# Kernel optimization log

Hardware: AMD Instinct MI355X
Metric: run time of the kernel (lower is better)

The kernel has to match this reference:

```python
import jax, jax.numpy as jnp
import numpy as np

B = 64
H = 768  # hidden_dim; x is [B, H, H], split along dim 1 into Q, D of [B, H//2, H]


def setup_inputs() -> dict:
    key = jax.random.key(0)
    kx, kw, kb = jax.random.split(key, 3)
    x = jax.random.normal(kx, (B, H, H), dtype=jnp.float32)
    # nn.Linear(H, H): weight [out, in], bias [out]
    W = jax.random.normal(kw, (H, H), dtype=jnp.float32) * (1.0 / np.sqrt(H))
    b = jax.random.normal(kb, (H,), dtype=jnp.float32) * 0.01
    return {"x": x, "W": W, "b": b}


def reference(x, W, b):
    T = H // 2
    Q = x[:, :T, :]          # [B, T, H]
    D = x[:, T:2 * T, :]     # [B, T, H]
    # Q = tanh(Linear(Q)); torch Linear: y = x @ W^T + b
    Q = jnp.tanh(jnp.einsum('bth,oh->bto', Q, W) + b)  # [B, T, H]
    D_t = jnp.swapaxes(D, 1, 2)                         # [B, H, T]
    L = jnp.einsum('bth,bsh->bts', Q, D)                # [B, T, T]
    A_Q = jnp.swapaxes(jax.nn.softmax(L, axis=1), 1, 2) # softmax over dim 1, then transpose -> [B, T, T]
    C_Q = jnp.matmul(D_t, A_Q)                          # [B, H, T]
    Q_t = jnp.swapaxes(Q, 1, 2)                         # [B, H, T]
    A_D = jax.nn.softmax(L, axis=2)                     # [B, T, T]
    C_D = jnp.matmul(jnp.concatenate((Q_t, C_Q), axis=1), A_D)  # [B, 2H, T]
    C_D_t = jnp.swapaxes(C_D, 1, 2)                     # [B, T, 2H]
    return jnp.concatenate((C_D_t, D), axis=2)          # [B, T, 3H]
```

## Files before the change

kernel.cpp:

```cpp
#include <hip/hip_runtime.h>


typedef __bf16 bf16x8 __attribute__((ext_vector_type(8)));
typedef __bf16 bf16x4 __attribute__((ext_vector_type(4)));
typedef float  f32x4  __attribute__((ext_vector_type(4)));

#define HH 768
#define TT 384

__device__ inline void split8(const float* __restrict__ p, bf16x8& hi, bf16x8& lo) {
    float4 f0 = *(const float4*)p;
    float4 f1 = *(const float4*)(p + 4);
    float f[8] = {f0.x, f0.y, f0.z, f0.w, f1.x, f1.y, f1.z, f1.w};
#pragma unroll
    for (int i = 0; i < 8; i++) {
        __bf16 h = (__bf16)f[i];
        hi[i] = h;
        lo[i] = (__bf16)(f[i] - (float)h);
    }
}

__device__ inline void gload16(const void* g, void* l) {
    __builtin_amdgcn_global_load_lds(
        (const __attribute__((address_space(1))) unsigned int*)g,
        (__attribute__((address_space(3))) unsigned int*)l, 16, 0, 0);
}

__global__ void prep_kernel(const float* __restrict__ x, __bf16* __restrict__ Dt,
                            float* __restrict__ out) {
    __shared__ float tile[32][33];
    int b = blockIdx.z;
    int h0 = blockIdx.x * 32, s0 = blockIdx.y * 32;
    int tx = threadIdx.x, ty = threadIdx.y;
    const float* src = x + ((size_t)b * HH + TT) * HH;
    float* outb = out + (size_t)b * TT * 2304;
#pragma unroll
    for (int j = 0; j < 4; j++) {
        int s = s0 + ty + 8 * j, h = h0 + tx;
        float v = src[(size_t)s * HH + h];
        tile[ty + 8 * j][tx] = v;
        outb[(size_t)s * 2304 + 1536 + h] = v;
    }
    __syncthreads();
    __bf16* Dtb = Dt + (size_t)b * HH * TT;
#pragma unroll
    for (int j = 0; j < 4; j++) {
        int h = h0 + ty + 8 * j, s = s0 + tx;
        Dtb[(size_t)h * TT + s] = (__bf16)tile[tx][ty + 8 * j];
    }
}

__global__ void splitW_kernel(const float* __restrict__ W, __bf16* __restrict__ Whi,
                              __bf16* __restrict__ Wlo) {
    int idx = blockIdx.x * 256 + threadIdx.x;
    bf16x8 h, l;
    split8(W + (size_t)idx * 8, h, l);
    *(bf16x8*)&Whi[(size_t)idx * 8] = h;
    *(bf16x8*)&Wlo[(size_t)idx * 8] = l;
}

__global__ __launch_bounds__(256) void gemm1_kernel(
    const float* __restrict__ x, const __bf16* __restrict__ Whi,
    const __bf16* __restrict__ Wlo, const float* __restrict__ bias,
    __bf16* __restrict__ Qhi, __bf16* __restrict__ Qlo, __bf16* __restrict__ M4) {
    __shared__ __bf16 Ah[128 * 32], Al[128 * 32], Bh[128 * 32], Bl[128 * 32];
    const int b = blockIdx.z;
    const int m_blk = blockIdx.y * 128, n_blk = blockIdx.x * 128;
    const int tid = threadIdx.x, lane = tid & 63, wave = tid >> 6;
    const int wm = wave >> 1, wn = wave & 1;
    const int r15 = lane & 15, quad = lane >> 4;
    const float* Abase = x + (size_t)b * HH * HH;
    f32x4 acc[4][4];
#pragma unroll
    for (int i = 0; i < 4; i++)
#pragma unroll
        for (int j = 0; j < 4; j++) acc[i][j] = (f32x4){0.f, 0.f, 0.f, 0.f};

    for (int k0 = 0; k0 < HH; k0 += 32) {
#pragma unroll
        for (int it = 0; it < 2; it++) {
            int c = it * 256 + tid;
            int r = c >> 2, q = c & 3;
            bf16x8 wh = *(const bf16x8*)&Whi[(size_t)(n_blk + r) * HH + k0 + q * 8];
            bf16x8 wl = *(const bf16x8*)&Wlo[(size_t)(n_blk + r) * HH + k0 + q * 8];
            *(bf16x8*)&Bh[c * 8] = wh;
            *(bf16x8*)&Bl[c * 8] = wl;
            bf16x8 h, l;
            split8(Abase + (size_t)(m_blk + r) * HH + k0 + q * 8, h, l);
            *(bf16x8*)&Ah[c * 8] = h;
            *(bf16x8*)&Al[c * 8] = l;
        }
        __syncthreads();
        bf16x8 ah[4], al[4], bh[4], bl[4];
#pragma unroll
        for (int i = 0; i < 4; i++) {
            int ra = (wm * 64 + i * 16 + r15) * 32 + quad * 8;
            ah[i] = *(const bf16x8*)&Ah[ra];
            al[i] = *(const bf16x8*)&Al[ra];
            int rb = (wn * 64 + i * 16 + r15) * 32 + quad * 8;
            bh[i] = *(const bf16x8*)&Bh[rb];
            bl[i] = *(const bf16x8*)&Bl[rb];
        }
#pragma unroll
        for (int i = 0; i < 4; i++)
#pragma unroll
            for (int j = 0; j < 4; j++) {
                acc[i][j] = __builtin_amdgcn_mfma_f32_16x16x32_bf16(ah[i], bh[j], acc[i][j], 0, 0, 0);
                acc[i][j] = __builtin_amdgcn_mfma_f32_16x16x32_bf16(ah[i], bl[j], acc[i][j], 0, 0, 0);
                acc[i][j] = __builtin_amdgcn_mfma_f32_16x16x32_bf16(al[i], bh[j], acc[i][j], 0, 0, 0);
            }
        __syncthreads();
    }
    __bf16* Qh = Qhi + (size_t)b * TT * HH;
    __bf16* Ql = Qlo + (size_t)b * TT * HH;
    __bf16* Mb = M4 + (size_t)b * 1536 * TT;
#pragma unroll
    for (int j = 0; j < 4; j++) {
        int col = n_blk + wn * 64 + j * 16 + r15;
        float bv = bias[col];
#pragma unroll
        for (int i = 0; i < 4; i++) {
            int row0 = m_blk + wm * 64 + i * 16 + quad * 4;
            bf16x4 mrow;
#pragma unroll
            for (int r = 0; r < 4; r++) {
                float v = tanhf(acc[i][j][r] + bv);
                __bf16 qh = (__bf16)v;
                Qh[(size_t)(row0 + r) * HH + col] = qh;
                Ql[(size_t)(row0 + r) * HH + col] = (__bf16)(v - (float)qh);
                mrow[r] = qh;
            }
            *(bf16x4*)&Mb[(size_t)col * TT + row0] = mrow;
        }
    }
}

__global__ __launch_bounds__(256) void gemm2_kernel(
    const __bf16* __restrict__ Qhi, const __bf16* __restrict__ Qlo,
    const float* __restrict__ x, float* __restrict__ L) {
    __shared__ __bf16 Ah[128 * 32], Al[128 * 32], Bh[128 * 32], Bl[128 * 32];
    const int b = blockIdx.z;
    const int m_blk = blockIdx.y * 128, n_blk = blockIdx.x * 128;
    const int tid = threadIdx.x, lane = tid & 63, wave = tid >> 6;
    const int wm = wave >> 1, wn = wave & 1;
    const int r15 = lane & 15, quad = lane >> 4;
    const __bf16* Qh = Qhi + (size_t)b * TT * HH;
    const __bf16* Ql = Qlo + (size_t)b * TT * HH;
    const float* Dbase = x + ((size_t)b * HH + TT) * HH;
    f32x4 acc[4][4];
#pragma unroll
    for (int i = 0; i < 4; i++)
#pragma unroll
        for (int j = 0; j < 4; j++) acc[i][j] = (f32x4){0.f, 0.f, 0.f, 0.f};

    for (int k0 = 0; k0 < HH; k0 += 32) {
#pragma unroll
        for (int it = 0; it < 2; it++) {
            int c = it * 256 + tid;
            int r = c >> 2, q = c & 3;
            bf16x8 qh8 = *(const bf16x8*)&Qh[(size_t)(m_blk + r) * HH + k0 + q * 8];
            bf16x8 ql8 = *(const bf16x8*)&Ql[(size_t)(m_blk + r) * HH + k0 + q * 8];
            *(bf16x8*)&Ah[c * 8] = qh8;
            *(bf16x8*)&Al[c * 8] = ql8;
            bf16x8 h, l;
            split8(Dbase + (size_t)(n_blk + r) * HH + k0 + q * 8, h, l);
            *(bf16x8*)&Bh[c * 8] = h;
            *(bf16x8*)&Bl[c * 8] = l;
        }
        __syncthreads();
        bf16x8 ah[4], al[4], bh[4], bl[4];
#pragma unroll
        for (int i = 0; i < 4; i++) {
            int ra = (wm * 64 + i * 16 + r15) * 32 + quad * 8;
            ah[i] = *(const bf16x8*)&Ah[ra];
            al[i] = *(const bf16x8*)&Al[ra];
            int rb = (wn * 64 + i * 16 + r15) * 32 + quad * 8;
            bh[i] = *(const bf16x8*)&Bh[rb];
            bl[i] = *(const bf16x8*)&Bl[rb];
        }
#pragma unroll
        for (int i = 0; i < 4; i++)
#pragma unroll
            for (int j = 0; j < 4; j++) {
                acc[i][j] = __builtin_amdgcn_mfma_f32_16x16x32_bf16(ah[i], bh[j], acc[i][j], 0, 0, 0);
                acc[i][j] = __builtin_amdgcn_mfma_f32_16x16x32_bf16(ah[i], bl[j], acc[i][j], 0, 0, 0);
                acc[i][j] = __builtin_amdgcn_mfma_f32_16x16x32_bf16(al[i], bh[j], acc[i][j], 0, 0, 0);
            }
        __syncthreads();
    }
    float* Lb = L + (size_t)b * TT * TT;
#pragma unroll
    for (int j = 0; j < 4; j++) {
        int col = n_blk + wn * 64 + j * 16 + r15;
#pragma unroll
        for (int i = 0; i < 4; i++) {
            int row0 = m_blk + wm * 64 + i * 16 + quad * 4;
#pragma unroll
            for (int r = 0; r < 4; r++) Lb[(size_t)(row0 + r) * TT + col] = acc[i][j][r];
        }
    }
}

__global__ void softmax_col_kernel(const float* __restrict__ L, __bf16* __restrict__ AQt) {
    int b = blockIdx.y;
    int tx = threadIdx.x, ty = threadIdx.y;
    int s = blockIdx.x * 64 + tx;
    const float* Lb = L + (size_t)b * TT * TT;
    __shared__ float red[4][64];
    float mx = -1e30f;
    for (int t = ty; t < TT; t += 4) mx = fmaxf(mx, Lb[(size_t)t * TT + s]);
    red[ty][tx] = mx;
    __syncthreads();
    mx = fmaxf(fmaxf(red[0][tx], red[1][tx]), fmaxf(red[2][tx], red[3][tx]));
    float sum = 0.f;
    for (int t = ty; t < TT; t += 4) sum += __expf(Lb[(size_t)t * TT + s] - mx);
    __syncthreads();
    red[ty][tx] = sum;
    __syncthreads();
    float inv = 1.0f / (red[0][tx] + red[1][tx] + red[2][tx] + red[3][tx]);
    __bf16* Ab = AQt + (size_t)b * TT * TT;
    for (int t = ty; t < TT; t += 4)
        Ab[(size_t)t * TT + s] = (__bf16)(__expf(Lb[(size_t)t * TT + s] - mx) * inv);
}

__global__ void softmax_row_kernel(const float* __restrict__ L, __bf16* __restrict__ ADt) {
    int b = blockIdx.y;
    int t0 = blockIdx.x * 64;
    int tx = threadIdx.x, ty = threadIdx.y;
    int tid = ty * 64 + tx;
    const float* Lb = L + (size_t)b * TT * TT;
    __shared__ __bf16 ex[64][TT];
    for (int rr = ty; rr < 64; rr += 4) {
        const float* row = Lb + (size_t)(t0 + rr) * TT;
        float v[6];
        float mx = -1e30f;
#pragma unroll
        for (int k = 0; k < 6; k++) {
            v[k] = row[tx + 64 * k];
            mx = fmaxf(mx, v[k]);
        }
#pragma unroll
        for (int off = 32; off > 0; off >>= 1) mx = fmaxf(mx, __shfl_xor(mx, off));
        float sum = 0.f;
#pragma unroll
        for (int k = 0; k < 6; k++) {
            v[k] = __expf(v[k] - mx);
            sum += v[k];
        }
#pragma unroll
        for (int off = 32; off > 0; off >>= 1) sum += __shfl_xor(sum, off);
        float inv = 1.0f / sum;
#pragma unroll
        for (int k = 0; k < 6; k++) ex[rr][tx + 64 * k] = (__bf16)(v[k] * inv);
    }
    __syncthreads();
    __bf16* Ab = ADt + (size_t)b * TT * TT;
    for (int s = tid; s < TT; s += 256) {
#pragma unroll
        for (int j = 0; j < 8; j++) {
            bf16x8 t8;
#pragma unroll
            for (int e = 0; e < 8; e++) t8[e] = ex[j * 8 + e][s];
            *(bf16x8*)&Ab[(size_t)s * TT + t0 + j * 8] = t8;
        }
    }
}

__global__ __launch_bounds__(256) void gemm3_kernel(
    const __bf16* __restrict__ Dt, const __bf16* __restrict__ AQt,
    __bf16* __restrict__ M4) {
    __shared__ __bf16 As[128 * 32], Bs[128 * 32];
    const int b = blockIdx.z;
    const int m_blk = blockIdx.y * 128, n_blk = blockIdx.x * 128;
    const int tid = threadIdx.x, lane = tid & 63, wave = tid >> 6;
    const int wm = wave >> 1, wn = wave & 1;
    const int r15 = lane & 15, quad = lane >> 4;
    const __bf16* Ab = Dt + (size_t)b * HH * TT;
    const __bf16* Bb = AQt + (size_t)b * TT * TT;
    f32x4 acc[4][4];
#pragma unroll
    for (int i = 0; i < 4; i++)
#pragma unroll
        for (int j = 0; j < 4; j++) acc[i][j] = (f32x4){0.f, 0.f, 0.f, 0.f};

    for (int k0 = 0; k0 < TT; k0 += 32) {
#pragma unroll
        for (int it = 0; it < 2; it++) {
            int c = it * 256 + tid;
            int r = c >> 2, q = c & 3;
            gload16(Ab + (size_t)(m_blk + r) * TT + k0 + q * 8, &As[c * 8]);
            gload16(Bb + (size_t)(n_blk + r) * TT + k0 + q * 8, &Bs[c * 8]);
        }
        __syncthreads();
        bf16x8 a[4], bf[4];
#pragma unroll
        for (int i = 0; i < 4; i++) {
            a[i] = *(const bf16x8*)&As[(wm * 64 + i * 16 + r15) * 32 + quad * 8];
            bf[i] = *(const bf16x8*)&Bs[(wn * 64 + i * 16 + r15) * 32 + quad * 8];
        }
#pragma unroll
        for (int i = 0; i < 4; i++)
#pragma unroll
            for (int j = 0; j < 4; j++)
                acc[i][j] = __builtin_amdgcn_mfma_f32_16x16x32_bf16(a[i], bf[j], acc[i][j], 0, 0, 0);
        __syncthreads();
    }
    __bf16* Mb = M4 + (size_t)b * 1536 * TT;
#pragma unroll
    for (int j = 0; j < 4; j++) {
        int col = n_blk + wn * 64 + j * 16 + r15;
#pragma unroll
        for (int i = 0; i < 4; i++) {
            int row0 = m_blk + wm * 64 + i * 16 + quad * 4;
#pragma unroll
            for (int r = 0; r < 4; r++)
                Mb[(size_t)(768 + row0 + r) * TT + col] = (__bf16)acc[i][j][r];
        }
    }
}

__global__ __launch_bounds__(256) void gemm4_kernel(
    const __bf16* __restrict__ ADt, const __bf16* __restrict__ M4,
    float* __restrict__ out) {
    __shared__ __bf16 As[128 * 32], Bs[128 * 32];
    const int b = blockIdx.z;
    const int m_blk = blockIdx.y * 128, n_blk = blockIdx.x * 128;
    const int tid = threadIdx.x, lane = tid & 63, wave = tid >> 6;
    const int wm = wave >> 1, wn = wave & 1;
    const int r15 = lane & 15, quad = lane >> 4;
    const __bf16* Ab = ADt + (size_t)b * TT * TT;
    const __bf16* Bb = M4 + (size_t)b * 1536 * TT;
    f32x4 acc[4][4];
#pragma unroll
    for (int i = 0; i < 4; i++)
#pragma unroll
        for (int j = 0; j < 4; j++) acc[i][j] = (f32x4){0.f, 0.f, 0.f, 0.f};

    for (int k0 = 0; k0 < TT; k0 += 32) {
#pragma unroll
        for (int it = 0; it < 2; it++) {
            int c = it * 256 + tid;
            int r = c >> 2, q = c & 3;
            gload16(Ab + (size_t)(m_blk + r) * TT + k0 + q * 8, &As[c * 8]);
            gload16(Bb + (size_t)(n_blk + r) * TT + k0 + q * 8, &Bs[c * 8]);
        }
        __syncthreads();
        bf16x8 a[4], bf[4];
#pragma unroll
        for (int i = 0; i < 4; i++) {
            a[i] = *(const bf16x8*)&As[(wm * 64 + i * 16 + r15) * 32 + quad * 8];
            bf[i] = *(const bf16x8*)&Bs[(wn * 64 + i * 16 + r15) * 32 + quad * 8];
        }
#pragma unroll
        for (int i = 0; i < 4; i++)
#pragma unroll
            for (int j = 0; j < 4; j++)
                acc[i][j] = __builtin_amdgcn_mfma_f32_16x16x32_bf16(a[i], bf[j], acc[i][j], 0, 0, 0);
        __syncthreads();
    }
    float* outb = out + (size_t)b * TT * 2304;
#pragma unroll
    for (int j = 0; j < 4; j++) {
        int col = n_blk + wn * 64 + j * 16 + r15;
#pragma unroll
        for (int i = 0; i < 4; i++) {
            int row0 = m_blk + wm * 64 + i * 16 + quad * 4;
#pragma unroll
            for (int r = 0; r < 4; r++)
                outb[(size_t)(row0 + r) * 2304 + col] = acc[i][j][r];
        }
    }
}

extern "C" void kernel_launch(void* const* d_in, const int* in_sizes, int n_in,
                              void* d_out, int out_size, void* d_ws, size_t ws_size,
                              hipStream_t stream) {
    const float* x = (const float*)d_in[0];
    const float* W = (const float*)d_in[1];
    const float* bias = (const float*)d_in[2];
    float* out = (float*)d_out;
    char* ws = (char*)d_ws;

    __bf16* Qhi = (__bf16*)(ws + 0);
    __bf16* Qlo = (__bf16*)(ws + 37748736);
    __bf16* M4 = (__bf16*)(ws + 75497472);
    __bf16* Dt = (__bf16*)(ws + 150994944);
    float* L = (float*)(ws + 188743680);
    __bf16* AQt = (__bf16*)(ws + 0);
    __bf16* ADt = (__bf16*)(ws + 37748736);
    __bf16* Whi = (__bf16*)(ws + 188743680);
    __bf16* Wlo = Whi + 768 * 768;

    prep_kernel<<<dim3(24, 12, 64), dim3(32, 8), 0, stream>>>(x, Dt, out);
    splitW_kernel<<<288, 256, 0, stream>>>(W, Whi, Wlo);
    gemm1_kernel<<<dim3(6, 3, 64), 256, 0, stream>>>(x, Whi, Wlo, bias, Qhi, Qlo, M4);
    gemm2_kernel<<<dim3(3, 3, 64), 256, 0, stream>>>(Qhi, Qlo, x, L);
    softmax_col_kernel<<<dim3(6, 64), dim3(64, 4), 0, stream>>>(L, AQt);
    softmax_row_kernel<<<dim3(6, 64), dim3(64, 4), 0, stream>>>(L, ADt);
    gemm3_kernel<<<dim3(3, 6, 64), 256, 0, stream>>>(Dt, AQt, M4);
    gemm4_kernel<<<dim3(12, 3, 64), 256, 0, stream>>>(ADt, M4, out);
}
```

Measured before the change: 815.8 us.

## Pre-split x and W into bf16 hi/lo scratch and stream via direct LDS loads

A new split kernel converts the Q half of x, the D half of x and W into bf16 hi/lo pairs once, storing them in spare regions of the output buffer and in workspace (M4, XQlo). gemm1 and gemm2 then fetch operands with global_load_lds directly into shared memory, no longer converting fp32 to bf16 inside every tile iteration. This removes repeated split work across the N-tiles and register staging of the loads. In exchange it adds an extra pass that writes and rereads scratch data, and it depends on later kernels overwriting the borrowed output regions and on M4 regions not being clobbered before use.

```diff
diff --git a/kernel.cpp b/kernel.cpp
--- a/kernel.cpp
+++ b/kernel.cpp
@@ -7,6 +7,7 @@
 
 #define HH 768
 #define TT 384
+#define OROWB 9216
 
 __device__ inline void split8(const float* __restrict__ p, bf16x8& hi, bf16x8& lo) {
     float4 f0 = *(const float4*)p;
@@ -50,18 +51,40 @@
     }
 }
 
-__global__ void splitW_kernel(const float* __restrict__ W, __bf16* __restrict__ Whi,
-                              __bf16* __restrict__ Wlo) {
+__global__ void splitX_kernel(const float* __restrict__ x, const float* __restrict__ W,
+                              char* __restrict__ outc, __bf16* __restrict__ M4,
+                              __bf16* __restrict__ XQlo) {
     int idx = blockIdx.x * 256 + threadIdx.x;
-    bf16x8 h, l;
-    split8(W + (size_t)idx * 8, h, l);
-    *(bf16x8*)&Whi[(size_t)idx * 8] = h;
-    *(bf16x8*)&Wlo[(size_t)idx * 8] = l;
+    const int NQ = 64 * 384 * 96;
+    if (idx < NQ) {
+        int hb = idx % 96, s = (idx / 96) % 384, b = idx / (96 * 384);
+        bf16x8 h, l;
+        split8(x + ((size_t)b * HH + s) * HH + hb * 8, h, l);
+        size_t o = (size_t)s * HH + hb * 8;
+        *(bf16x8*)&M4[((size_t)b * 1536 + 768) * TT + o] = h;
+        *(bf16x8*)&XQlo[(size_t)b * TT * HH + o] = l;
+    } else if (idx < 2 * NQ) {
+        int j = idx - NQ;
+        int hb = j % 96, s = (j / 96) % 384, b = j / (96 * 384);
+        bf16x8 h, l;
+        split8(x + ((size_t)b * HH + TT + s) * HH + hb * 8, h, l);
+        char* p = outc + (size_t)b * TT * OROWB + (size_t)s * OROWB + hb * 16;
+        *(bf16x8*)(p + 3072) = h;
+        *(bf16x8*)(p + 4608) = l;
+    } else {
+        int wi = idx - 2 * NQ;
+        int hb = wi % 96, o = wi / 96;
+        bf16x8 h, l;
+        split8(W + (size_t)o * HH + hb * 8, h, l);
+        char* p = outc + (size_t)o * OROWB + hb * 16;
+        *(bf16x8*)p = h;
+        *(bf16x8*)(p + 1536) = l;
+    }
 }
 
 __global__ __launch_bounds__(256) void gemm1_kernel(
-    const float* __restrict__ x, const __bf16* __restrict__ Whi,
-    const __bf16* __restrict__ Wlo, const float* __restrict__ bias,
+    const __bf16* __restrict__ XQlo, const char* __restrict__ wscr,
+    const float* __restrict__ bias,
     __bf16* __restrict__ Qhi, __bf16* __restrict__ Qlo, __bf16* __restrict__ M4) {
     __shared__ __bf16 Ah[128 * 32], Al[128 * 32], Bh[128 * 32], Bl[128 * 32];
     const int b = blockIdx.z;
@@ -69,7 +92,8 @@
     const int tid = threadIdx.x, lane = tid & 63, wave = tid >> 6;
     const int wm = wave >> 1, wn = wave & 1;
     const int r15 = lane & 15, quad = lane >> 4;
-    const float* Abase = x + (size_t)b * HH * HH;
+    const __bf16* XQh = M4 + ((size_t)b * 1536 + 768) * TT;
+    const __bf16* XQl = XQlo + (size_t)b * TT * HH;
     f32x4 acc[4][4];
 #pragma unroll
     for (int i = 0; i < 4; i++)
@@ -81,14 +105,11 @@
         for (int it = 0; it < 2; it++) {
             int c = it * 256 + tid;
             int r = c >> 2, q = c & 3;
-            bf16x8 wh = *(const bf16x8*)&Whi[(size_t)(n_blk + r) * HH + k0 + q * 8];
-            bf16x8 wl = *(const bf16x8*)&Wlo[(size_t)(n_blk + r) * HH + k0 + q * 8];
-            *(bf16x8*)&Bh[c * 8] = wh;
-            *(bf16x8*)&Bl[c * 8] = wl;
-            bf16x8 h, l;
-            split8(Abase + (size_t)(m_blk + r) * HH + k0 + q * 8, h, l);
-            *(bf16x8*)&Ah[c * 8] = h;
-            *(bf16x8*)&Al[c * 8] = l;
+            gload16(XQh + (size_t)(m_blk + r) * HH + k0 + q * 8, &Ah[c * 8]);
+            gload16(XQl + (size_t)(m_blk + r) * HH + k0 + q * 8, &Al[c * 8]);
+            const char* wrow = wscr + (size_t)(n_blk + r) * OROWB + (size_t)(k0 + q * 8) * 2;
+            gload16(wrow, &Bh[c * 8]);
+            gload16(wrow + 1536, &Bl[c * 8]);
         }
         __syncthreads();
         bf16x8 ah[4], al[4], bh[4], bl[4];
@@ -137,7 +158,7 @@
 
 __global__ __launch_bounds__(256) void gemm2_kernel(
     const __bf16* __restrict__ Qhi, const __bf16* __restrict__ Qlo,
-    const float* __restrict__ x, float* __restrict__ L) {
+    const char* __restrict__ outscr, float* __restrict__ L) {
     __shared__ __bf16 Ah[128 * 32], Al[128 * 32], Bh[128 * 32], Bl[128 * 32];
     const int b = blockIdx.z;
     const int m_blk = blockIdx.y * 128, n_blk = blockIdx.x * 128;
@@ -146,7 +167,7 @@
     const int r15 = lane & 15, quad = lane >> 4;
     const __bf16* Qh = Qhi + (size_t)b * TT * HH;
     const __bf16* Ql = Qlo + (size_t)b * TT * HH;
-    const float* Dbase = x + ((size_t)b * HH + TT) * HH;
+    const char* scr = outscr + (size_t)b * TT * OROWB;
     f32x4 acc[4][4];
 #pragma unroll
     for (int i = 0; i < 4; i++)
@@ -158,14 +179,11 @@
         for (int it = 0; it < 2; it++) {
             int c = it * 256 + tid;
             int r = c >> 2, q = c & 3;
-            bf16x8 qh8 = *(const bf16x8*)&Qh[(size_t)(m_blk + r) * HH + k0 + q * 8];
-            bf16x8 ql8 = *(const bf16x8*)&Ql[(size_t)(m_blk + r) * HH + k0 + q * 8];
-            *(bf16x8*)&Ah[c * 8] = qh8;
-            *(bf16x8*)&Al[c * 8] = ql8;
-            bf16x8 h, l;
-            split8(Dbase + (size_t)(n_blk + r) * HH + k0 + q * 8, h, l);
-            *(bf16x8*)&Bh[c * 8] = h;
-            *(bf16x8*)&Bl[c * 8] = l;
+            gload16(Qh + (size_t)(m_blk + r) * HH + k0 + q * 8, &Ah[c * 8]);
+            gload16(Ql + (size_t)(m_blk + r) * HH + k0 + q * 8, &Al[c * 8]);
+            const char* drow = scr + (size_t)(n_blk + r) * OROWB + (size_t)(k0 + q * 8) * 2;
+            gload16(drow + 3072, &Bh[c * 8]);
+            gload16(drow + 4608, &Bl[c * 8]);
         }
         __syncthreads();
         bf16x8 ah[4], al[4], bh[4], bl[4];
@@ -388,13 +406,12 @@
     float* L = (float*)(ws + 188743680);
     __bf16* AQt = (__bf16*)(ws + 0);
     __bf16* ADt = (__bf16*)(ws + 37748736);
-    __bf16* Whi = (__bf16*)(ws + 188743680);
-    __bf16* Wlo = Whi + 768 * 768;
+    __bf16* XQlo = (__bf16*)(ws + 188743680);
 
     prep_kernel<<<dim3(24, 12, 64), dim3(32, 8), 0, stream>>>(x, Dt, out);
-    splitW_kernel<<<288, 256, 0, stream>>>(W, Whi, Wlo);
-    gemm1_kernel<<<dim3(6, 3, 64), 256, 0, stream>>>(x, Whi, Wlo, bias, Qhi, Qlo, M4);
-    gemm2_kernel<<<dim3(3, 3, 64), 256, 0, stream>>>(Qhi, Qlo, x, L);
+    splitX_kernel<<<18720, 256, 0, stream>>>(x, W, (char*)out, M4, XQlo);
+    gemm1_kernel<<<dim3(6, 3, 64), 256, 0, stream>>>(XQlo, (const char*)out, bias, Qhi, Qlo, M4);
+    gemm2_kernel<<<dim3(3, 3, 64), 256, 0, stream>>>(Qhi, Qlo, (const char*)out, L);
     softmax_col_kernel<<<dim3(6, 64), dim3(64, 4), 0, stream>>>(L, AQt);
     softmax_row_kernel<<<dim3(6, 64), dim3(64, 4), 0, stream>>>(L, ADt);
     gemm3_kernel<<<dim3(3, 6, 64), 256, 0, stream>>>(Dt, AQt, M4);
```

Measured after the change: 869.1 us. 1.07x slower.

## Software-pipeline gemm1 and gemm2 with register prefetch and async LDS double buffering

Applied to the files above, without the earlier changes.

In both split-bf16 GEMMs, the fp32 operand for the next K-slice is now prefetched into registers and split into hi/lo only after the current slice is consumed. The pre-split bf16 operand is loaded straight into a double-buffered LDS tile with global_load_lds, issued one iteration ahead. The aim is to hide global-memory latency behind the MFMA work of the current slice. The cost is extra LDS and registers, which may lower occupancy, and correctness relies on the barriers waiting for the async LDS loads.

```diff
diff --git a/kernel.cpp b/kernel.cpp
--- a/kernel.cpp
+++ b/kernel.cpp
@@ -11,6 +11,16 @@
 __device__ inline void split8(const float* __restrict__ p, bf16x8& hi, bf16x8& lo) {
     float4 f0 = *(const float4*)p;
     float4 f1 = *(const float4*)(p + 4);
+    float f[8] = {f0.x, f0.y, f0.z, f0.w, f1.x, f1.y, f1.z, f1.w};
+#pragma unroll
+    for (int i = 0; i < 8; i++) {
+        __bf16 h = (__bf16)f[i];
+        hi[i] = h;
+        lo[i] = (__bf16)(f[i] - (float)h);
+    }
+}
+
+__device__ inline void split8r(float4 f0, float4 f1, bf16x8& hi, bf16x8& lo) {
     float f[8] = {f0.x, f0.y, f0.z, f0.w, f1.x, f1.y, f1.z, f1.w};
 #pragma unroll
     for (int i = 0; i < 8; i++) {
@@ -63,34 +73,57 @@
     const float* __restrict__ x, const __bf16* __restrict__ Whi,
     const __bf16* __restrict__ Wlo, const float* __restrict__ bias,
     __bf16* __restrict__ Qhi, __bf16* __restrict__ Qlo, __bf16* __restrict__ M4) {
-    __shared__ __bf16 Ah[128 * 32], Al[128 * 32], Bh[128 * 32], Bl[128 * 32];
+    __shared__ __bf16 Ah[128 * 32], Al[128 * 32];
+    __shared__ __bf16 Bh[2][128 * 32], Bl[2][128 * 32];
     const int b = blockIdx.z;
     const int m_blk = blockIdx.y * 128, n_blk = blockIdx.x * 128;
     const int tid = threadIdx.x, lane = tid & 63, wave = tid >> 6;
     const int wm = wave >> 1, wn = wave & 1;
     const int r15 = lane & 15, quad = lane >> 4;
     const float* Abase = x + (size_t)b * HH * HH;
+    const int ra0 = tid >> 2, qa = tid & 3;
+    const float* aptr0 = Abase + (size_t)(m_blk + ra0) * HH + qa * 8;
+    const float* aptr1 = Abase + (size_t)(m_blk + ra0 + 64) * HH + qa * 8;
     f32x4 acc[4][4];
 #pragma unroll
     for (int i = 0; i < 4; i++)
 #pragma unroll
         for (int j = 0; j < 4; j++) acc[i][j] = (f32x4){0.f, 0.f, 0.f, 0.f};
 
+    float4 a00 = *(const float4*)(aptr0);
+    float4 a01 = *(const float4*)(aptr0 + 4);
+    float4 a10 = *(const float4*)(aptr1);
+    float4 a11 = *(const float4*)(aptr1 + 4);
+#pragma unroll
+    for (int it = 0; it < 2; it++) {
+        int c = it * 256 + tid, r = c >> 2, q = c & 3;
+        gload16(Whi + (size_t)(n_blk + r) * HH + q * 8, &Bh[0][c * 8]);
+        gload16(Wlo + (size_t)(n_blk + r) * HH + q * 8, &Bl[0][c * 8]);
+    }
+    int cur = 0;
     for (int k0 = 0; k0 < HH; k0 += 32) {
-#pragma unroll
-        for (int it = 0; it < 2; it++) {
-            int c = it * 256 + tid;
-            int r = c >> 2, q = c & 3;
-            bf16x8 wh = *(const bf16x8*)&Whi[(size_t)(n_blk + r) * HH + k0 + q * 8];
-            bf16x8 wl = *(const bf16x8*)&Wlo[(size_t)(n_blk + r) * HH + k0 + q * 8];
-            *(bf16x8*)&Bh[c * 8] = wh;
-            *(bf16x8*)&Bl[c * 8] = wl;
+        {
             bf16x8 h, l;
-            split8(Abase + (size_t)(m_blk + r) * HH + k0 + q * 8, h, l);
-            *(bf16x8*)&Ah[c * 8] = h;
-            *(bf16x8*)&Al[c * 8] = l;
-        }
-        __syncthreads();
+            split8r(a00, a01, h, l);
+            *(bf16x8*)&Ah[tid * 8] = h;
+            *(bf16x8*)&Al[tid * 8] = l;
+            split8r(a10, a11, h, l);
+            *(bf16x8*)&Ah[(256 + tid) * 8] = h;
+            *(bf16x8*)&Al[(256 + tid) * 8] = l;
+        }
+        __syncthreads();
+        if (k0 + 32 < HH) {
+            a00 = *(const float4*)(aptr0 + k0 + 32);
+            a01 = *(const float4*)(aptr0 + k0 + 36);
+            a10 = *(const float4*)(aptr1 + k0 + 32);
+            a11 = *(const float4*)(aptr1 + k0 + 36);
+#pragma unroll
+            for (int it = 0; it < 2; it++) {
+                int c = it * 256 + tid, r = c >> 2, q = c & 3;
+                gload16(Whi + (size_t)(n_blk + r) * HH + k0 + 32 + q * 8, &Bh[cur ^ 1][c * 8]);
+                gload16(Wlo + (size_t)(n_blk + r) * HH + k0 + 32 + q * 8, &Bl[cur ^ 1][c * 8]);
+            }
+        }
         bf16x8 ah[4], al[4], bh[4], bl[4];
 #pragma unroll
         for (int i = 0; i < 4; i++) {
@@ -98,8 +131,8 @@
             ah[i] = *(const bf16x8*)&Ah[ra];
             al[i] = *(const bf16x8*)&Al[ra];
             int rb = (wn * 64 + i * 16 + r15) * 32 + quad * 8;
-            bh[i] = *(const bf16x8*)&Bh[rb];
-            bl[i] = *(const bf16x8*)&Bl[rb];
+            bh[i] = *(const bf16x8*)&Bh[cur][rb];
+            bl[i] = *(const bf16x8*)&Bl[cur][rb];
         }
 #pragma unroll
         for (int i = 0; i < 4; i++)
@@ -110,6 +143,7 @@
                 acc[i][j] = __builtin_amdgcn_mfma_f32_16x16x32_bf16(al[i], bh[j], acc[i][j], 0, 0, 0);
             }
         __syncthreads();
+        cur ^= 1;
     }
     __bf16* Qh = Qhi + (size_t)b * TT * HH;
     __bf16* Ql = Qlo + (size_t)b * TT * HH;
@@ -138,7 +172,8 @@
 __global__ __launch_bounds__(256) void gemm2_kernel(
     const __bf16* __restrict__ Qhi, const __bf16* __restrict__ Qlo,
     const float* __restrict__ x, float* __restrict__ L) {
-    __shared__ __bf16 Ah[128 * 32], Al[128 * 32], Bh[128 * 32], Bl[128 * 32];
+    __shared__ __bf16 Ah[2][128 * 32], Al[2][128 * 32];
+    __shared__ __bf16 Bh[128 * 32], Bl[128 * 32];
     const int b = blockIdx.z;
     const int m_blk = blockIdx.y * 128, n_blk = blockIdx.x * 128;
     const int tid = threadIdx.x, lane = tid & 63, wave = tid >> 6;
@@ -147,33 +182,55 @@
     const __bf16* Qh = Qhi + (size_t)b * TT * HH;
     const __bf16* Ql = Qlo + (size_t)b * TT * HH;
     const float* Dbase = x + ((size_t)b * HH + TT) * HH;
+    const int rb0 = tid >> 2, qb = tid & 3;
+    const float* dptr0 = Dbase + (size_t)(n_blk + rb0) * HH + qb * 8;
+    const float* dptr1 = Dbase + (size_t)(n_blk + rb0 + 64) * HH + qb * 8;
     f32x4 acc[4][4];
 #pragma unroll
     for (int i = 0; i < 4; i++)
 #pragma unroll
         for (int j = 0; j < 4; j++) acc[i][j] = (f32x4){0.f, 0.f, 0.f, 0.f};
 
+    float4 d00 = *(const float4*)(dptr0);
+    float4 d01 = *(const float4*)(dptr0 + 4);
+    float4 d10 = *(const float4*)(dptr1);
+    float4 d11 = *(const float4*)(dptr1 + 4);
+#pragma unroll
+    for (int it = 0; it < 2; it++) {
+        int c = it * 256 + tid, r = c >> 2, q = c & 3;
+        gload16(Qh + (size_t)(m_blk + r) * HH + q * 8, &Ah[0][c * 8]);
+        gload16(Ql + (size_t)(m_blk + r) * HH + q * 8, &Al[0][c * 8]);
+    }
+    int cur = 0;
     for (int k0 = 0; k0 < HH; k0 += 32) {
-#pragma unroll
-        for (int it = 0; it < 2; it++) {
-            int c = it * 256 + tid;
-            int r = c >> 2, q = c & 3;
-            bf16x8 qh8 = *(const bf16x8*)&Qh[(size_t)(m_blk + r) * HH + k0 + q * 8];
-            bf16x8 ql8 = *(const bf16x8*)&Ql[(size_t)(m_blk + r) * HH + k0 + q * 8];
-            *(bf16x8*)&Ah[c * 8] = qh8;
-            *(bf16x8*)&Al[c * 8] = ql8;
+        {
             bf16x8 h, l;
-            split8(Dbase + (size_t)(n_blk + r) * HH + k0 + q * 8, h, l);
-            *(bf16x8*)&Bh[c * 8] = h;
-            *(bf16x8*)&Bl[c * 8] = l;
-        }
-        __syncthreads();
+            split8r(d00, d01, h, l);
+            *(bf16x8*)&Bh[tid * 8] = h;
+            *(bf16x8*)&Bl[tid * 8] = l;
+            split8r(d10, d11, h, l);
+            *(bf16x8*)&Bh[(256 + tid) * 8] = h;
+            *(bf16x8*)&Bl[(256 + tid) * 8] = l;
+        }
+        __syncthreads();
+        if (k0 + 32 < HH) {
+            d00 = *(const float4*)(dptr0 + k0 + 32);
+            d01 = *(const float4*)(dptr0 + k0 + 36);
+            d10 = *(const float4*)(dptr1 + k0 + 32);
+            d11 = *(const float4*)(dptr1 + k0 + 36);
+#pragma unroll
+            for (int it = 0; it < 2; it++) {
+                int c = it * 256 + tid, r = c >> 2, q = c & 3;
+                gload16(Qh + (size_t)(m_blk + r) * HH + k0 + 32 + q * 8, &Ah[cur ^ 1][c * 8]);
+                gload16(Ql + (size_t)(m_blk + r) * HH + k0 + 32 + q * 8, &Al[cur ^ 1][c * 8]);
+            }
+        }
         bf16x8 ah[4], al[4], bh[4], bl[4];
 #pragma unroll
         for (int i = 0; i < 4; i++) {
             int ra = (wm * 64 + i * 16 + r15) * 32 + quad * 8;
-            ah[i] = *(const bf16x8*)&Ah[ra];
-            al[i] = *(const bf16x8*)&Al[ra];
+            ah[i] = *(const bf16x8*)&Ah[cur][ra];
+            al[i] = *(const bf16x8*)&Al[cur][ra];
             int rb = (wn * 64 + i * 16 + r15) * 32 + quad * 8;
             bh[i] = *(const bf16x8*)&Bh[rb];
             bl[i] = *(const bf16x8*)&Bl[rb];
@@ -187,6 +244,7 @@
                 acc[i][j] = __builtin_amdgcn_mfma_f32_16x16x32_bf16(al[i], bh[j], acc[i][j], 0, 0, 0);
             }
         __syncthreads();
+        cur ^= 1;
     }
     float* Lb = L + (size_t)b * TT * TT;
 #pragma unroll
```

Measured after the change: 797.9 us. -2.2%, faster.
